# Kernel tuning notes

Measured on AMD Instinct MI355X. Metric: run time of the kernel, lower is better.

## Reference

```python
import jax, jax.numpy as jnp
import numpy as np

STD = 1.0  # components_std from cfg
LOG_2PI = float(np.log(2.0 * np.pi))


def setup_inputs() -> dict:
    key = jax.random.key(0)
    k1, k2, k3 = jax.random.split(key, 3)
    B, S, D, K = 256, 1024, 32, 512
    x = jax.random.normal(k1, (B, S, D), dtype=jnp.float32)
    logits = jax.random.normal(k2, (B, K), dtype=jnp.float32)
    # xavier_normal_ init on (K, D): std = sqrt(2 / (K + D))
    means = jax.random.normal(k3, (K, D), dtype=jnp.float32) * np.sqrt(2.0 / (K + D))
    return {"x": x, "logits": logits, "means": means}


def reference(x, logits, means):
    # x: [B, S, D], logits: [B, K], means: [K, D]
    D = x.shape[-1]
    log_mix = jax.nn.log_softmax(logits, axis=-1)  # [B, K] Categorical log-probs
    # squared distance ||x - mu||^2 via expansion (avoids [B,S,K,D] intermediate)
    x2 = jnp.sum(x * x, axis=-1)          # [B, S]
    m2 = jnp.sum(means * means, axis=-1)  # [K]
    xm = jnp.einsum('bsd,kd->bsk', x, means)  # [B, S, K]
    sq = x2[..., None] - 2.0 * xm + m2        # [B, S, K]
    inv_var = 1.0 / (STD * STD)
    log_norm = D * (jnp.log(jnp.float32(STD)) + 0.5 * LOG_2PI)
    comp_logpdf = -0.5 * inv_var * sq - log_norm  # [B, S, K] Independent-Normal logpdf
    # mixture log_prob = logsumexp over components; NLL = negative
    nll = -jax.nn.logsumexp(log_mix[:, None, :] + comp_logpdf, axis=-1)  # [B, S]
    return nll
```

## Files before the change

### kernel.cpp

```cpp
#include <hip/hip_runtime.h>
#include <math.h>

constexpr int Bc = 256, Sc = 1024, Dc = 32, Kc = 512;
constexpr int ST = 128;
constexpr float LOG2E    = 1.4426950408889634f;
constexpr float LN2      = 0.6931471805599453f;
constexpr float LOG_NORM = 29.40603306051f;

typedef __attribute__((ext_vector_type(8))) short          bf16x8;
typedef __attribute__((ext_vector_type(8))) unsigned short u16x8;
typedef __attribute__((ext_vector_type(4))) float          f32x4;

#if __has_builtin(__builtin_amdgcn_exp2f)
#define EXP2F(v) __builtin_amdgcn_exp2f(v)
#else
#define EXP2F(v) exp2f(v)
#endif
#if __has_builtin(__builtin_amdgcn_logf)
#define LOG2F(v) __builtin_amdgcn_logf(v)
#else
#define LOG2F(v) log2f(v)
#endif

__device__ __forceinline__ unsigned short f2bf(float f) {
    unsigned u = __float_as_uint(f);
    u += 0x7fff + ((u >> 16) & 1);
    return (unsigned short)(u >> 16);
}

__device__ __forceinline__ int swz(int row, int chunk) {
    return row * 32 + ((chunk ^ ((row >> 1) & 3)) << 3);
}

__global__ __launch_bounds__(256)
void gm_prep(const float* __restrict__ logits, const float* __restrict__ means,
             float* __restrict__ wbuf, unsigned short* __restrict__ mbf)
{
    __shared__ float red[8];
    const int tid  = threadIdx.x;
    const int lane = tid & 63;
    const int wid  = tid >> 6;
    const int b    = blockIdx.x;

    const float l0 = logits[b * Kc + tid];
    const float l1 = logits[b * Kc + tid + 256];
    float mx = fmaxf(l0, l1);
    #pragma unroll
    for (int off = 32; off >= 1; off >>= 1) mx = fmaxf(mx, __shfl_xor(mx, off));
    if (lane == 0) red[wid] = mx;
    __syncthreads();
    mx = fmaxf(fmaxf(red[0], red[1]), fmaxf(red[2], red[3]));
    float sm = EXP2F((l0 - mx) * LOG2E) + EXP2F((l1 - mx) * LOG2E);
    #pragma unroll
    for (int off = 32; off >= 1; off >>= 1) sm += __shfl_xor(sm, off);
    if (lane == 0) red[4 + wid] = sm;
    __syncthreads();
    sm = red[4] + red[5] + red[6] + red[7];
    const float lse = mx + LN2 * LOG2F(sm);

    #pragma unroll
    for (int rr = 0; rr < 2; ++rr) {
        const int k = tid + rr * 256;
        const float4* mp = (const float4*)(means + (size_t)k * Dc);
        float m2 = 0.f;
        #pragma unroll
        for (int i = 0; i < 8; ++i) {
            float4 v = mp[i];
            m2 += v.x*v.x + v.y*v.y + v.z*v.z + v.w*v.w;
        }
        const float lg = (rr == 0) ? l0 : l1;
        wbuf[(size_t)b * Kc + k] = EXP2F((lg - lse - 0.5f * m2) * LOG2E);
    }

    if (tid < 64) {
        const int row = 2 * b + (tid >> 5);
        const int col = tid & 31;
        mbf[row * 32 + col] = f2bf(means[(size_t)row * 32 + col]);
    }
}

__global__ __launch_bounds__(256)
void gm_main(const float* __restrict__ x, const float* __restrict__ wbuf,
             const unsigned short* __restrict__ mbf, float* __restrict__ out)
{
    __shared__ unsigned short mlds[Kc * 32];
    __shared__ float wlds[Kc];
    __shared__ float x2p[ST];

    const int tid  = threadIdx.x;
    const int lane = tid & 63;
    const int wid  = tid >> 6;
    const int b    = blockIdx.x >> 3;
    const int s0   = (blockIdx.x & 7) * ST;
    const int q    = lane >> 4;
    const int ln   = lane & 15;
    const int rw   = wid * 32;

    {
        const u16x8* src = (const u16x8*)mbf;
        #pragma unroll
        for (int j = 0; j < 8; ++j) {
            const int c = tid + j * 256;
            *(u16x8*)&mlds[swz(c >> 2, c & 3)] = src[c];
        }
        wlds[tid]       = wbuf[(size_t)b * Kc + tid];
        wlds[tid + 256] = wbuf[(size_t)b * Kc + tid + 256];
    }

    const int row0 = rw + ln, row1 = row0 + 16;
    const float4* xp0 = (const float4*)(x + ((size_t)b * Sc + s0 + row0) * Dc) + q * 2;
    const float4* xp1 = (const float4*)(x + ((size_t)b * Sc + s0 + row1) * Dc) + q * 2;
    float4 v0 = xp0[0], v1 = xp0[1];
    float4 u0 = xp1[0], u1 = xp1[1];

    bf16x8 a0, a1;
    a0[0]=(short)f2bf(v0.x*LOG2E); a0[1]=(short)f2bf(v0.y*LOG2E);
    a0[2]=(short)f2bf(v0.z*LOG2E); a0[3]=(short)f2bf(v0.w*LOG2E);
    a0[4]=(short)f2bf(v1.x*LOG2E); a0[5]=(short)f2bf(v1.y*LOG2E);
    a0[6]=(short)f2bf(v1.z*LOG2E); a0[7]=(short)f2bf(v1.w*LOG2E);
    a1[0]=(short)f2bf(u0.x*LOG2E); a1[1]=(short)f2bf(u0.y*LOG2E);
    a1[2]=(short)f2bf(u0.z*LOG2E); a1[3]=(short)f2bf(u0.w*LOG2E);
    a1[4]=(short)f2bf(u1.x*LOG2E); a1[5]=(short)f2bf(u1.y*LOG2E);
    a1[6]=(short)f2bf(u1.z*LOG2E); a1[7]=(short)f2bf(u1.w*LOG2E);

    float p0 = v0.x*v0.x + v0.y*v0.y + v0.z*v0.z + v0.w*v0.w
             + v1.x*v1.x + v1.y*v1.y + v1.z*v1.z + v1.w*v1.w;
    float p1 = u0.x*u0.x + u0.y*u0.y + u0.z*u0.z + u0.w*u0.w
             + u1.x*u1.x + u1.y*u1.y + u1.z*u1.z + u1.w*u1.w;
    p0 += __shfl_xor(p0, 16); p0 += __shfl_xor(p0, 32);
    p1 += __shfl_xor(p1, 16); p1 += __shfl_xor(p1, 32);
    if (q == 0) { x2p[row0] = p0; x2p[row1] = p1; }
    __syncthreads();

    const f32x4 zero = {0.f, 0.f, 0.f, 0.f};
    float acc0[4] = {0.f, 0.f, 0.f, 0.f};
    float acc1[4] = {0.f, 0.f, 0.f, 0.f};

    #pragma unroll 8
    for (int kt = 0; kt < 32; ++kt) {
        const int krow = kt * 16 + ln;
        const bf16x8 bfr = *(const bf16x8*)&mlds[swz(krow, q)];
        const float  wv  = wlds[krow];
        f32x4 d0 = __builtin_amdgcn_mfma_f32_16x16x32_bf16(a0, bfr, zero, 0, 0, 0);
        f32x4 d1 = __builtin_amdgcn_mfma_f32_16x16x32_bf16(a1, bfr, zero, 0, 0, 0);
        #pragma unroll
        for (int r = 0; r < 4; ++r) {
            acc0[r] = fmaf(wv, EXP2F(d0[r]), acc0[r]);
            acc1[r] = fmaf(wv, EXP2F(d1[r]), acc1[r]);
        }
    }

    #pragma unroll
    for (int r = 0; r < 4; ++r) {
        float s0v = acc0[r], s1v = acc1[r];
        s0v += __shfl_xor(s0v, 1); s0v += __shfl_xor(s0v, 2);
        s0v += __shfl_xor(s0v, 4); s0v += __shfl_xor(s0v, 8);
        s1v += __shfl_xor(s1v, 1); s1v += __shfl_xor(s1v, 2);
        s1v += __shfl_xor(s1v, 4); s1v += __shfl_xor(s1v, 8);
        if (ln == 0) {
            const int r0 = rw + q * 4 + r;
            const int r1 = r0 + 16;
            out[(size_t)b * Sc + s0 + r0] = 0.5f * x2p[r0] + LOG_NORM - LN2 * LOG2F(s0v);
            out[(size_t)b * Sc + s0 + r1] = 0.5f * x2p[r1] + LOG_NORM - LN2 * LOG2F(s1v);
        }
    }
}

extern "C" void kernel_launch(void* const* d_in, const int* in_sizes, int n_in,
                              void* d_out, int out_size, void* d_ws, size_t ws_size,
                              hipStream_t stream) {
    const float* x      = (const float*)d_in[0];
    const float* logits = (const float*)d_in[1];
    const float* means  = (const float*)d_in[2];
    float* out = (float*)d_out;
    (void)in_sizes; (void)n_in; (void)out_size; (void)ws_size;

    unsigned short* mbf  = (unsigned short*)d_ws;
    float*          wbuf = (float*)((char*)d_ws + 32768);

    hipLaunchKernelGGL(gm_prep, dim3(Bc), dim3(256), 0, stream,
                       logits, means, wbuf, mbf);
    hipLaunchKernelGGL(gm_main, dim3(Bc * (Sc / ST)), dim3(256), 0, stream,
                       x, wbuf, mbf, out);
}
```

Baseline: 95.26 us.

## Double rows per block in main kernel and restructure prep means handling

The main kernel now processes 256 sequence rows per block (4 MFMA row-tiles per wave instead of 2), halving the number of blocks and the number of times the bf16 means table and weights are loaded into LDS. This amortizes per-block staging cost. The prep kernel now stages per-chunk squared norms of all means in shared memory, and block 0 alone converts the full means table to bf16. The risk is that every prep block rereads the whole means array, and the larger per-thread accumulator state raises register pressure, which the launch bound of 4 blocks per CU tries to cap.

```diff
diff --git a/kernel.cpp b/kernel.cpp
--- a/kernel.cpp
+++ b/kernel.cpp
@@ -2,13 +2,14 @@
 #include <math.h>
 
 constexpr int Bc = 256, Sc = 1024, Dc = 32, Kc = 512;
-constexpr int ST = 128;
+constexpr int ST = 256;
 constexpr float LOG2E    = 1.4426950408889634f;
 constexpr float LN2      = 0.6931471805599453f;
 constexpr float LOG_NORM = 29.40603306051f;
 
 typedef __attribute__((ext_vector_type(8))) short          bf16x8;
 typedef __attribute__((ext_vector_type(8))) unsigned short u16x8;
+typedef __attribute__((ext_vector_type(4))) unsigned short u16x4;
 typedef __attribute__((ext_vector_type(4))) float          f32x4;
 
 #if __has_builtin(__builtin_amdgcn_exp2f)
@@ -36,11 +37,25 @@
 void gm_prep(const float* __restrict__ logits, const float* __restrict__ means,
              float* __restrict__ wbuf, unsigned short* __restrict__ mbf)
 {
+    __shared__ float csum[4096];
     __shared__ float red[8];
     const int tid  = threadIdx.x;
     const int lane = tid & 63;
     const int wid  = tid >> 6;
     const int b    = blockIdx.x;
+
+    const float4* m4 = (const float4*)means;
+    #pragma unroll
+    for (int j = 0; j < 16; ++j) {
+        const int i = tid + j * 256;
+        float4 v = m4[i];
+        csum[i] = v.x*v.x + v.y*v.y + v.z*v.z + v.w*v.w;
+        if (b == 0) {
+            u16x4 pk;
+            pk[0] = f2bf(v.x); pk[1] = f2bf(v.y); pk[2] = f2bf(v.z); pk[3] = f2bf(v.w);
+            *(u16x4*)&mbf[i * 4] = pk;
+        }
+    }
 
     const float l0 = logits[b * Kc + tid];
     const float l1 = logits[b * Kc + tid + 256];
@@ -61,25 +76,15 @@
     #pragma unroll
     for (int rr = 0; rr < 2; ++rr) {
         const int k = tid + rr * 256;
-        const float4* mp = (const float4*)(means + (size_t)k * Dc);
-        float m2 = 0.f;
-        #pragma unroll
-        for (int i = 0; i < 8; ++i) {
-            float4 v = mp[i];
-            m2 += v.x*v.x + v.y*v.y + v.z*v.z + v.w*v.w;
-        }
+        const float* cs = &csum[k * 8];
+        float m2 = ((cs[0] + cs[1]) + (cs[2] + cs[3]))
+                 + ((cs[4] + cs[5]) + (cs[6] + cs[7]));
         const float lg = (rr == 0) ? l0 : l1;
         wbuf[(size_t)b * Kc + k] = EXP2F((lg - lse - 0.5f * m2) * LOG2E);
     }
-
-    if (tid < 64) {
-        const int row = 2 * b + (tid >> 5);
-        const int col = tid & 31;
-        mbf[row * 32 + col] = f2bf(means[(size_t)row * 32 + col]);
-    }
 }
 
-__global__ __launch_bounds__(256)
+__global__ __launch_bounds__(256, 4)
 void gm_main(const float* __restrict__ x, const float* __restrict__ wbuf,
              const unsigned short* __restrict__ mbf, float* __restrict__ out)
 {
@@ -90,11 +95,11 @@
     const int tid  = threadIdx.x;
     const int lane = tid & 63;
     const int wid  = tid >> 6;
-    const int b    = blockIdx.x >> 3;
-    const int s0   = (blockIdx.x & 7) * ST;
+    const int b    = blockIdx.x >> 2;
+    const int s0   = (blockIdx.x & 3) * ST;
     const int q    = lane >> 4;
     const int ln   = lane & 15;
-    const int rw   = wid * 32;
+    const int rw   = wid * 64;
 
     {
         const u16x8* src = (const u16x8*)mbf;
@@ -107,61 +112,56 @@
         wlds[tid + 256] = wbuf[(size_t)b * Kc + tid + 256];
     }
 
-    const int row0 = rw + ln, row1 = row0 + 16;
-    const float4* xp0 = (const float4*)(x + ((size_t)b * Sc + s0 + row0) * Dc) + q * 2;
-    const float4* xp1 = (const float4*)(x + ((size_t)b * Sc + s0 + row1) * Dc) + q * 2;
-    float4 v0 = xp0[0], v1 = xp0[1];
-    float4 u0 = xp1[0], u1 = xp1[1];
-
-    bf16x8 a0, a1;
-    a0[0]=(short)f2bf(v0.x*LOG2E); a0[1]=(short)f2bf(v0.y*LOG2E);
-    a0[2]=(short)f2bf(v0.z*LOG2E); a0[3]=(short)f2bf(v0.w*LOG2E);
-    a0[4]=(short)f2bf(v1.x*LOG2E); a0[5]=(short)f2bf(v1.y*LOG2E);
-    a0[6]=(short)f2bf(v1.z*LOG2E); a0[7]=(short)f2bf(v1.w*LOG2E);
-    a1[0]=(short)f2bf(u0.x*LOG2E); a1[1]=(short)f2bf(u0.y*LOG2E);
-    a1[2]=(short)f2bf(u0.z*LOG2E); a1[3]=(short)f2bf(u0.w*LOG2E);
-    a1[4]=(short)f2bf(u1.x*LOG2E); a1[5]=(short)f2bf(u1.y*LOG2E);
-    a1[6]=(short)f2bf(u1.z*LOG2E); a1[7]=(short)f2bf(u1.w*LOG2E);
-
-    float p0 = v0.x*v0.x + v0.y*v0.y + v0.z*v0.z + v0.w*v0.w
-             + v1.x*v1.x + v1.y*v1.y + v1.z*v1.z + v1.w*v1.w;
-    float p1 = u0.x*u0.x + u0.y*u0.y + u0.z*u0.z + u0.w*u0.w
-             + u1.x*u1.x + u1.y*u1.y + u1.z*u1.z + u1.w*u1.w;
-    p0 += __shfl_xor(p0, 16); p0 += __shfl_xor(p0, 32);
-    p1 += __shfl_xor(p1, 16); p1 += __shfl_xor(p1, 32);
-    if (q == 0) { x2p[row0] = p0; x2p[row1] = p1; }
+    bf16x8 a[4];
+    #pragma unroll
+    for (int t = 0; t < 4; ++t) {
+        const int row = rw + 16 * t + ln;
+        const float4* xp = (const float4*)(x + ((size_t)b * Sc + s0 + row) * Dc) + q * 2;
+        float4 v0 = xp[0], v1 = xp[1];
+        a[t][0]=(short)f2bf(v0.x*LOG2E); a[t][1]=(short)f2bf(v0.y*LOG2E);
+        a[t][2]=(short)f2bf(v0.z*LOG2E); a[t][3]=(short)f2bf(v0.w*LOG2E);
+        a[t][4]=(short)f2bf(v1.x*LOG2E); a[t][5]=(short)f2bf(v1.y*LOG2E);
+        a[t][6]=(short)f2bf(v1.z*LOG2E); a[t][7]=(short)f2bf(v1.w*LOG2E);
+        float p = v0.x*v0.x + v0.y*v0.y + v0.z*v0.z + v0.w*v0.w
+                + v1.x*v1.x + v1.y*v1.y + v1.z*v1.z + v1.w*v1.w;
+        p += __shfl_xor(p, 16); p += __shfl_xor(p, 32);
+        if (q == 0) x2p[row] = p;
+    }
     __syncthreads();
 
     const f32x4 zero = {0.f, 0.f, 0.f, 0.f};
-    float acc0[4] = {0.f, 0.f, 0.f, 0.f};
-    float acc1[4] = {0.f, 0.f, 0.f, 0.f};
+    float acc[4][4] = {};
 
-    #pragma unroll 8
+    #pragma unroll 4
     for (int kt = 0; kt < 32; ++kt) {
         const int krow = kt * 16 + ln;
         const bf16x8 bfr = *(const bf16x8*)&mlds[swz(krow, q)];
         const float  wv  = wlds[krow];
-        f32x4 d0 = __builtin_amdgcn_mfma_f32_16x16x32_bf16(a0, bfr, zero, 0, 0, 0);
-        f32x4 d1 = __builtin_amdgcn_mfma_f32_16x16x32_bf16(a1, bfr, zero, 0, 0, 0);
+        f32x4 d0 = __builtin_amdgcn_mfma_f32_16x16x32_bf16(a[0], bfr, zero, 0, 0, 0);
+        f32x4 d1 = __builtin_amdgcn_mfma_f32_16x16x32_bf16(a[1], bfr, zero, 0, 0, 0);
+        f32x4 d2 = __builtin_amdgcn_mfma_f32_16x16x32_bf16(a[2], bfr, zero, 0, 0, 0);
+        f32x4 d3 = __builtin_amdgcn_mfma_f32_16x16x32_bf16(a[3], bfr, zero, 0, 0, 0);
         #pragma unroll
         for (int r = 0; r < 4; ++r) {
-            acc0[r] = fmaf(wv, EXP2F(d0[r]), acc0[r]);
-            acc1[r] = fmaf(wv, EXP2F(d1[r]), acc1[r]);
+            acc[0][r] = fmaf(wv, EXP2F(d0[r]), acc[0][r]);
+            acc[1][r] = fmaf(wv, EXP2F(d1[r]), acc[1][r]);
+            acc[2][r] = fmaf(wv, EXP2F(d2[r]), acc[2][r]);
+            acc[3][r] = fmaf(wv, EXP2F(d3[r]), acc[3][r]);
         }
     }
 
     #pragma unroll
-    for (int r = 0; r < 4; ++r) {
-        float s0v = acc0[r], s1v = acc1[r];
-        s0v += __shfl_xor(s0v, 1); s0v += __shfl_xor(s0v, 2);
-        s0v += __shfl_xor(s0v, 4); s0v += __shfl_xor(s0v, 8);
-        s1v += __shfl_xor(s1v, 1); s1v += __shfl_xor(s1v, 2);
-        s1v += __shfl_xor(s1v, 4); s1v += __shfl_xor(s1v, 8);
-        if (ln == 0) {
-            const int r0 = rw + q * 4 + r;
-            const int r1 = r0 + 16;
-            out[(size_t)b * Sc + s0 + r0] = 0.5f * x2p[r0] + LOG_NORM - LN2 * LOG2F(s0v);
-            out[(size_t)b * Sc + s0 + r1] = 0.5f * x2p[r1] + LOG_NORM - LN2 * LOG2F(s1v);
+    for (int t = 0; t < 4; ++t) {
+        #pragma unroll
+        for (int r = 0; r < 4; ++r) {
+            float v = acc[t][r];
+            v += __shfl_xor(v, 1); v += __shfl_xor(v, 2);
+            v += __shfl_xor(v, 4); v += __shfl_xor(v, 8);
+            if (ln == 0) {
+                const int row = rw + 16 * t + q * 4 + r;
+                out[(size_t)b * Sc + s0 + row] =
+                    0.5f * x2p[row] + LOG_NORM - LN2 * LOG2F(v);
+            }
         }
     }
 }
```

After: 97.26 us. 2.1% more time.

## Fold log-softmax into main kernel and shrink prep to means conversion

Applied to the files above, without the earlier changes.

The per-batch prep kernel, which computed the log-softmax and per-component weights for every batch row, is replaced by a tiny 64-block kernel that only converts the means to bf16 and computes their squared norms. The main kernel now computes the weights exp(logit - 0.5*m2) and the log-sum-exp of the logits itself, and adds the normaliser once per output instead of folding it into each weight. This shrinks the serial prep stage before the main kernel. The cost is that each of the 8 blocks per batch row repeats the log-softmax reduction and adds a barrier.

```diff
diff --git a/kernel.cpp b/kernel.cpp
--- a/kernel.cpp
+++ b/kernel.cpp
@@ -33,59 +33,28 @@
 }
 
 __global__ __launch_bounds__(256)
-void gm_prep(const float* __restrict__ logits, const float* __restrict__ means,
-             float* __restrict__ wbuf, unsigned short* __restrict__ mbf)
+void gm_m2bf(const float* __restrict__ means,
+             unsigned short* __restrict__ mbf, float* __restrict__ m2buf)
 {
-    __shared__ float red[8];
-    const int tid  = threadIdx.x;
-    const int lane = tid & 63;
-    const int wid  = tid >> 6;
-    const int b    = blockIdx.x;
-
-    const float l0 = logits[b * Kc + tid];
-    const float l1 = logits[b * Kc + tid + 256];
-    float mx = fmaxf(l0, l1);
+    const int i    = blockIdx.x * 256 + threadIdx.x;
+    const int lane = threadIdx.x & 63;
+    const float v  = means[i];
+    mbf[i] = f2bf(v);
+    float sq = v * v;
     #pragma unroll
-    for (int off = 32; off >= 1; off >>= 1) mx = fmaxf(mx, __shfl_xor(mx, off));
-    if (lane == 0) red[wid] = mx;
-    __syncthreads();
-    mx = fmaxf(fmaxf(red[0], red[1]), fmaxf(red[2], red[3]));
-    float sm = EXP2F((l0 - mx) * LOG2E) + EXP2F((l1 - mx) * LOG2E);
-    #pragma unroll
-    for (int off = 32; off >= 1; off >>= 1) sm += __shfl_xor(sm, off);
-    if (lane == 0) red[4 + wid] = sm;
-    __syncthreads();
-    sm = red[4] + red[5] + red[6] + red[7];
-    const float lse = mx + LN2 * LOG2F(sm);
-
-    #pragma unroll
-    for (int rr = 0; rr < 2; ++rr) {
-        const int k = tid + rr * 256;
-        const float4* mp = (const float4*)(means + (size_t)k * Dc);
-        float m2 = 0.f;
-        #pragma unroll
-        for (int i = 0; i < 8; ++i) {
-            float4 v = mp[i];
-            m2 += v.x*v.x + v.y*v.y + v.z*v.z + v.w*v.w;
-        }
-        const float lg = (rr == 0) ? l0 : l1;
-        wbuf[(size_t)b * Kc + k] = EXP2F((lg - lse - 0.5f * m2) * LOG2E);
-    }
-
-    if (tid < 64) {
-        const int row = 2 * b + (tid >> 5);
-        const int col = tid & 31;
-        mbf[row * 32 + col] = f2bf(means[(size_t)row * 32 + col]);
-    }
+    for (int off = 1; off <= 16; off <<= 1) sq += __shfl_xor(sq, off);
+    if ((lane & 31) == 0) m2buf[i >> 5] = sq;
 }
 
 __global__ __launch_bounds__(256)
-void gm_main(const float* __restrict__ x, const float* __restrict__ wbuf,
-             const unsigned short* __restrict__ mbf, float* __restrict__ out)
+void gm_main(const float* __restrict__ x, const float* __restrict__ logits,
+             const float* __restrict__ m2buf, const unsigned short* __restrict__ mbf,
+             float* __restrict__ out)
 {
     __shared__ unsigned short mlds[Kc * 32];
     __shared__ float wlds[Kc];
     __shared__ float x2p[ST];
+    __shared__ float red[8];
 
     const int tid  = threadIdx.x;
     const int lane = tid & 63;
@@ -103,9 +72,17 @@
             const int c = tid + j * 256;
             *(u16x8*)&mlds[swz(c >> 2, c & 3)] = src[c];
         }
-        wlds[tid]       = wbuf[(size_t)b * Kc + tid];
-        wlds[tid + 256] = wbuf[(size_t)b * Kc + tid + 256];
     }
+
+    const float l0 = logits[b * Kc + tid];
+    const float l1 = logits[b * Kc + tid + 256];
+    wlds[tid]       = EXP2F((l0 - 0.5f * m2buf[tid])       * LOG2E);
+    wlds[tid + 256] = EXP2F((l1 - 0.5f * m2buf[tid + 256]) * LOG2E);
+
+    float mx = fmaxf(l0, l1);
+    #pragma unroll
+    for (int off = 32; off >= 1; off >>= 1) mx = fmaxf(mx, __shfl_xor(mx, off));
+    if (lane == 0) red[wid] = mx;
 
     const int row0 = rw + ln, row1 = row0 + 16;
     const float4* xp0 = (const float4*)(x + ((size_t)b * Sc + s0 + row0) * Dc) + q * 2;
@@ -132,6 +109,12 @@
     if (q == 0) { x2p[row0] = p0; x2p[row1] = p1; }
     __syncthreads();
 
+    const float mxb = fmaxf(fmaxf(red[0], red[1]), fmaxf(red[2], red[3]));
+    float sm = EXP2F((l0 - mxb) * LOG2E) + EXP2F((l1 - mxb) * LOG2E);
+    #pragma unroll
+    for (int off = 32; off >= 1; off >>= 1) sm += __shfl_xor(sm, off);
+    if (lane == 0) red[4 + wid] = sm;
+
     const f32x4 zero = {0.f, 0.f, 0.f, 0.f};
     float acc0[4] = {0.f, 0.f, 0.f, 0.f};
     float acc1[4] = {0.f, 0.f, 0.f, 0.f};
@@ -149,6 +132,9 @@
             acc1[r] = fmaf(wv, EXP2F(d1[r]), acc1[r]);
         }
     }
+    __syncthreads();
+    const float lse = mxb + LN2 * LOG2F(red[4] + red[5] + red[6] + red[7]);
+    const float base = LOG_NORM + lse;
 
     #pragma unroll
     for (int r = 0; r < 4; ++r) {
@@ -160,8 +146,8 @@
         if (ln == 0) {
             const int r0 = rw + q * 4 + r;
             const int r1 = r0 + 16;
-            out[(size_t)b * Sc + s0 + r0] = 0.5f * x2p[r0] + LOG_NORM - LN2 * LOG2F(s0v);
-            out[(size_t)b * Sc + s0 + r1] = 0.5f * x2p[r1] + LOG_NORM - LN2 * LOG2F(s1v);
+            out[(size_t)b * Sc + s0 + r0] = 0.5f * x2p[r0] + base - LN2 * LOG2F(s0v);
+            out[(size_t)b * Sc + s0 + r1] = 0.5f * x2p[r1] + base - LN2 * LOG2F(s1v);
         }
     }
 }
@@ -175,11 +161,10 @@
     float* out = (float*)d_out;
     (void)in_sizes; (void)n_in; (void)out_size; (void)ws_size;
 
-    unsigned short* mbf  = (unsigned short*)d_ws;
-    float*          wbuf = (float*)((char*)d_ws + 32768);
+    unsigned short* mbf   = (unsigned short*)d_ws;
+    float*          m2buf = (float*)((char*)d_ws + 32768);
 
-    hipLaunchKernelGGL(gm_prep, dim3(Bc), dim3(256), 0, stream,
-                       logits, means, wbuf, mbf);
+    hipLaunchKernelGGL(gm_m2bf, dim3(64), dim3(256), 0, stream, means, mbf, m2buf);
     hipLaunchKernelGGL(gm_main, dim3(Bc * (Sc / ST)), dim3(256), 0, stream,
-                       x, wbuf, mbf, out);
+                       x, logits, m2buf, mbf, out);
 }
```

Result: no change. 94.66 us (-0.6%).
